# Kernel optimization log

Hardware: AMD Instinct MI355X
Metric: run time of the kernel (lower is better)

Reference implementation:

```python
import jax, jax.numpy as jnp
import numpy as np

B, S, DIM = 1, 4096, 4096
H, HL, D = 32, 8, 128          # query heads, kv heads (GQA), head_dim
BS = 8                          # sparse_block_size
SINK_TOK, WIN_TOK = 30, 30
HEAVY = 800                     # heavy_const -> Mb = HEAVY // BS top blocks
NEG = -1e30


def setup_inputs() -> dict:
    key = jax.random.key(0)
    k0, k1, k2, k3 = jax.random.split(key, 4)
    x = jax.random.normal(k0, (B, S, DIM), jnp.float32)
    freqs_cis = jax.random.uniform(k1, (S, D // 2, 2), jnp.float32)  # (cos,sin)-like pairs
    wqkv_w = jax.random.normal(k2, ((H + 2 * HL) * D, DIM), jnp.float32) * 0.02
    wo_w = jax.random.normal(k3, (DIM, DIM), jnp.float32) * 0.02
    input_pos = jnp.arange(S, dtype=jnp.int32)
    return {"x": x, "freqs_cis": freqs_cis, "wqkv_w": wqkv_w, "wo_w": wo_w, "input_pos": input_pos}


def _rope(x, fc):
    # x: [B,S,h,D], fc: [S,D/2,2]
    xr = x.reshape(*x.shape[:-1], -1, 2)            # [B,S,h,D/2,2]
    fc = fc[None, :, None]                           # [1,S,1,D/2,2]
    out = jnp.stack([xr[..., 0] * fc[..., 0] - xr[..., 1] * fc[..., 1],
                     xr[..., 1] * fc[..., 0] + xr[..., 0] * fc[..., 1]], axis=-1)
    return out.reshape(x.shape)


def reference(x, freqs_cis, wqkv_w, wo_w, input_pos):
    rep = H // HL
    Tb = (S + BS - 1) // BS
    scale = 1.0 / jnp.sqrt(jnp.float32(D))

    qkv = x @ wqkv_w.T                               # [B,S,(H+2HL)*D]
    q, k, v = jnp.split(qkv, [H * D, (H + HL) * D], axis=-1)
    q = q.reshape(B, S, H, D)
    k = k.reshape(B, S, HL, D)
    v = v.reshape(B, S, HL, D)
    q = _rope(q, freqs_cis)
    k = _rope(k, freqs_cis)

    # ---- block accumulators (KVCache.update_tokens), vectorized ----
    blk = input_pos // BS                            # [S]
    k_sum = jax.ops.segment_sum(jnp.swapaxes(k, 0, 1), blk, num_segments=Tb)  # [Tb,B,HL,D]
    cnt = jax.ops.segment_sum(jnp.ones((S,), jnp.float32), blk, num_segments=Tb)  # [Tb]
    k_rep = k_sum / jnp.maximum(cnt, 1.0)[:, None, None, None]                # block-mean keys
    k_rep_h = jnp.repeat(k_rep, rep, axis=2)        # [Tb,B,H,D] (GQA repeat)

    # ---- per-(B,H) block routing scores ----
    q_mean = q.mean(axis=1)                          # [B,H,D]
    scores = jnp.einsum('bhd,tbhd->bht', q_mean, k_rep_h) * scale  # [B,H,Tb]
    scores = jnp.where(cnt[None, None, :] > 0, scores, NEG)

    # ---- build_block_index: sink + window + topk ----
    sink_b = min((min(SINK_TOK, S) + BS - 1) // BS, Tb)
    window_b = min((min(WIN_TOK, S) + BS - 1) // BS, Tb)
    cur_block = (S - 1) // BS
    win_start = max(0, cur_block - window_b + 1)
    win_end = cur_block + 1
    sink_ids = jnp.arange(sink_b, dtype=jnp.int32)
    window_ids = jnp.arange(win_start, win_end, dtype=jnp.int32)
    Mb = max(0, min(HEAVY // BS, Tb))
    sc = scores.at[..., :sink_b].set(NEG).at[..., window_ids].set(NEG)
    top_ids = jax.lax.top_k(sc, Mb)[1].astype(jnp.int32)                      # [B,H,Mb]
    bidx = jnp.concatenate([
        jnp.broadcast_to(sink_ids, (B, H, sink_b)),
        jnp.broadcast_to(window_ids, (B, H, win_end - win_start)),
        top_ids], axis=-1)                           # [B,H,KLIST]

    # ---- gather selected block tokens ----
    tok = bidx[..., None] * BS + jnp.arange(BS, dtype=jnp.int32)              # [B,H,KLIST,BS]
    KL = bidx.shape[-1]
    tok = tok.reshape(B, H, KL * BS)                 # [B,H,Kt]
    valid = (tok >= 0) & (tok < S)
    tok_c = jnp.clip(tok, 0, S - 1)

    k_bhsd = jnp.swapaxes(jnp.repeat(k, rep, axis=2), 1, 2)  # [B,H,S,D]
    v_bhsd = jnp.swapaxes(jnp.repeat(v, rep, axis=2), 1, 2)
    Ksel = jnp.take_along_axis(k_bhsd, tok_c[..., None], axis=2)  # [B,H,Kt,D]
    Vsel = jnp.take_along_axis(v_bhsd, tok_c[..., None], axis=2)

    # ---- block-sparse attention with causal mask ----
    q_bhsd = jnp.swapaxes(q, 1, 2)                   # [B,H,S,D]
    att = jnp.einsum('bhsd,bhkd->bhsk', q_bhsd, Ksel) * scale
    mask = (tok_c[:, :, None, :] <= input_pos[None, None, :, None]) & valid[:, :, None, :]
    att = jnp.where(mask, att, NEG)
    p = jax.nn.softmax(att, axis=-1)
    out = jnp.einsum('bhsk,bhkd->bhsd', p, Vsel)     # [B,H,S,D]
    y = jnp.swapaxes(out, 1, 2).reshape(B, S, H * D) @ wo_w.T
    return y
```

## Files before the change

kernel.cpp:

```cpp
#include <hip/hip_runtime.h>
#include <hip/hip_bf16.h>

typedef unsigned short u16;
typedef unsigned int   u32;

using bf16x8 = __attribute__((ext_vector_type(8))) short;
using f32x4  = __attribute__((ext_vector_type(4))) float;

constexpr int S = 4096, DIM = 4096, H = 32, HL = 8, D = 128;
constexpr int NQKV = (H + 2 * HL) * D;
constexpr int TB = S / 8;
constexpr int KL = 108;
constexpr float NEGF = -1e30f;
constexpr float SCALE = 0.08838834764831845f;

__device__ inline float bflo(u32 u) { return __builtin_bit_cast(float, u << 16); }
__device__ inline float bfhi(u32 u) { return __builtin_bit_cast(float, u & 0xFFFF0000u); }
__device__ inline u16 rne16(float f) {
  u32 b = __builtin_bit_cast(u32, f);
  return (u16)((b + 0x7FFFu + ((b >> 16) & 1u)) >> 16);
}
__device__ inline float bf2f(u16 h) { return __builtin_bit_cast(float, (u32)h << 16); }
__device__ inline u32 pk2(u16 a, u16 b) { return (u32)a | ((u32)b << 16); }

__device__ __forceinline__ void gload16(const u16* g, u16* l) {
  __builtin_amdgcn_global_load_lds(
      (__attribute__((address_space(1))) void*)g,
      (__attribute__((address_space(3))) void*)l, 16, 0, 0);
}

__global__ __launch_bounds__(256) void split_f32_kernel(
    const float* __restrict__ src, u16* __restrict__ hi, u16* __restrict__ lo) {
  const size_t i = ((size_t)blockIdx.x * 256 + threadIdx.x) * 8;
  float4 v0 = *(const float4*)(src + i);
  float4 v1 = *(const float4*)(src + i + 4);
  float f[8] = {v0.x, v0.y, v0.z, v0.w, v1.x, v1.y, v1.z, v1.w};
  u16 h[8], l[8];
#pragma unroll
  for (int j = 0; j < 8; ++j) {
    h[j] = rne16(f[j]);
    l[j] = rne16(f[j] - bf2f(h[j]));
  }
  uint4 ph, pl;
  ph.x = pk2(h[0], h[1]); ph.y = pk2(h[2], h[3]);
  ph.z = pk2(h[4], h[5]); ph.w = pk2(h[6], h[7]);
  pl.x = pk2(l[0], l[1]); pl.y = pk2(l[2], l[3]);
  pl.z = pk2(l[4], l[5]); pl.w = pk2(l[6], l[7]);
  *(uint4*)(hi + i) = ph;
  *(uint4*)(lo + i) = pl;
}

__global__ __launch_bounds__(256) void conv_wqkv_kernel(
    const float* __restrict__ src, u16* __restrict__ dst, u16* __restrict__ klo) {
  const size_t i = ((size_t)blockIdx.x * 256 + threadIdx.x) * 8;
  float4 v0 = *(const float4*)(src + i);
  float4 v1 = *(const float4*)(src + i + 4);
  float f[8] = {v0.x, v0.y, v0.z, v0.w, v1.x, v1.y, v1.z, v1.w};
  u16 h[8];
#pragma unroll
  for (int j = 0; j < 8; ++j) h[j] = rne16(f[j]);
  uint4 ph;
  ph.x = pk2(h[0], h[1]); ph.y = pk2(h[2], h[3]);
  ph.z = pk2(h[4], h[5]); ph.w = pk2(h[6], h[7]);
  *(uint4*)(dst + i) = ph;
  const int row = (int)(i >> 12);
  if (row >= H * D && row < (H + HL) * D) {
    u16 l[8];
#pragma unroll
    for (int j = 0; j < 8; ++j) l[j] = rne16(f[j] - bf2f(h[j]));
    uint4 pl;
    pl.x = pk2(l[0], l[1]); pl.y = pk2(l[2], l[3]);
    pl.z = pk2(l[4], l[5]); pl.w = pk2(l[6], l[7]);
    *(uint4*)(klo + (i - (size_t)(H * D) * DIM)) = pl;
  }
}

__global__ __launch_bounds__(256) void cast_bf16_kernel(
    const float* __restrict__ src, u16* __restrict__ dst) {
  const size_t i = ((size_t)blockIdx.x * 256 + threadIdx.x) * 8;
  float4 v0 = *(const float4*)(src + i);
  float4 v1 = *(const float4*)(src + i + 4);
  uint4 ph;
  ph.x = pk2(rne16(v0.x), rne16(v0.y));
  ph.y = pk2(rne16(v0.z), rne16(v0.w));
  ph.z = pk2(rne16(v1.x), rne16(v1.y));
  ph.w = pk2(rne16(v1.z), rne16(v1.w));
  *(uint4*)(dst + i) = ph;
}

template <bool OBF16>
__global__ __launch_bounds__(256) void gemm_bf16(
    const u16* __restrict__ A, const u16* __restrict__ B,
    void* __restrict__ Cp, int M, int N, int K, int lda, int ldb, int ldc) {
  __shared__ u16 As[128 * 32];
  __shared__ u16 Bs[128 * 32];
  const int tid = threadIdx.x;
  const int lane = tid & 63;
  const int w = tid >> 6;
  const int wm = w >> 1, wn = w & 1;
  const int m0 = blockIdx.y * 128, n0 = blockIdx.x * 128;
  const int l15 = lane & 15, g = lane >> 4;
  const int srow = tid >> 2;
  const int scol = (tid & 3) * 8;

  const u16* ga = A + (size_t)(m0 + srow) * lda + scol;
  const u16* gb = B + (size_t)(n0 + srow) * ldb + scol;
  const size_t a64 = (size_t)64 * lda;
  const size_t b64 = (size_t)64 * ldb;
  u16* lA = As + w * 512;
  u16* lB = Bs + w * 512;

  f32x4 acc[4][4];
#pragma unroll
  for (int i = 0; i < 4; ++i)
#pragma unroll
    for (int j = 0; j < 4; ++j) acc[i][j] = {0.f, 0.f, 0.f, 0.f};

  for (int k0 = 0; k0 < K; k0 += 32) {
    gload16(ga + k0, lA);
    gload16(ga + k0 + a64, lA + 2048);
    gload16(gb + k0, lB);
    gload16(gb + k0 + b64, lB + 2048);
    __syncthreads();
    bf16x8 af[4], bfr[4];
#pragma unroll
    for (int i = 0; i < 4; ++i)
      af[i] = *(const bf16x8*)(As + (wm * 64 + i * 16 + l15) * 32 + g * 8);
#pragma unroll
    for (int j = 0; j < 4; ++j)
      bfr[j] = *(const bf16x8*)(Bs + (wn * 64 + j * 16 + l15) * 32 + g * 8);
#pragma unroll
    for (int i = 0; i < 4; ++i)
#pragma unroll
      for (int j = 0; j < 4; ++j)
        acc[i][j] = __builtin_amdgcn_mfma_f32_16x16x32_bf16(af[i], bfr[j], acc[i][j], 0, 0, 0);
    __syncthreads();
  }
#pragma unroll
  for (int i = 0; i < 4; ++i)
#pragma unroll
    for (int j = 0; j < 4; ++j)
#pragma unroll
      for (int rg = 0; rg < 4; ++rg) {
        const int row = m0 + wm * 64 + i * 16 + g * 4 + rg;
        const int col = n0 + wn * 64 + j * 16 + l15;
        if constexpr (OBF16)
          ((u16*)Cp)[(size_t)row * ldc + col] = rne16(acc[i][j][rg]);
        else
          ((float*)Cp)[(size_t)row * ldc + col] = acc[i][j][rg];
      }
}

__global__ __launch_bounds__(256) void gemm_k3(
    const u16* __restrict__ Ahg, const u16* __restrict__ Alg,
    const u16* __restrict__ Bhg, const u16* __restrict__ Blg,
    float* __restrict__ C, int M, int N, int K) {
  __shared__ u16 Ah[128 * 32];
  __shared__ u16 Al[128 * 32];
  __shared__ u16 Bh[64 * 32];
  __shared__ u16 Bl[64 * 32];
  const int tid = threadIdx.x;
  const int lane = tid & 63;
  const int w = tid >> 6;
  const int wm = w >> 1, wn = w & 1;
  const int m0 = blockIdx.y * 128, n0 = blockIdx.x * 64;
  const int l15 = lane & 15, g = lane >> 4;
  const int srow = tid >> 2;
  const int scol = (tid & 3) * 8;

  const u16* gah = Ahg + (size_t)(m0 + srow) * K + scol;
  const u16* gal = Alg + (size_t)(m0 + srow) * K + scol;
  const u16* gbh = Bhg + (size_t)(n0 + srow) * K + scol;
  const u16* gbl = Blg + (size_t)(n0 + srow) * K + scol;
  const size_t a64 = (size_t)64 * K;
  u16* lAh = Ah + w * 512;
  u16* lAl = Al + w * 512;
  u16* lBh = Bh + w * 512;
  u16* lBl = Bl + w * 512;

  f32x4 acc[4][2];
#pragma unroll
  for (int i = 0; i < 4; ++i)
#pragma unroll
    for (int j = 0; j < 2; ++j) acc[i][j] = {0.f, 0.f, 0.f, 0.f};

  for (int k0 = 0; k0 < K; k0 += 32) {
    gload16(gah + k0, lAh);
    gload16(gah + k0 + a64, lAh + 2048);
    gload16(gal + k0, lAl);
    gload16(gal + k0 + a64, lAl + 2048);
    gload16(gbh + k0, lBh);
    gload16(gbl + k0, lBl);
    __syncthreads();
    bf16x8 fah[4], fal[4], fbh[2], fbl[2];
#pragma unroll
    for (int i = 0; i < 4; ++i) {
      fah[i] = *(const bf16x8*)(Ah + (wm * 64 + i * 16 + l15) * 32 + g * 8);
      fal[i] = *(const bf16x8*)(Al + (wm * 64 + i * 16 + l15) * 32 + g * 8);
    }
#pragma unroll
    for (int j = 0; j < 2; ++j) {
      fbh[j] = *(const bf16x8*)(Bh + (wn * 32 + j * 16 + l15) * 32 + g * 8);
      fbl[j] = *(const bf16x8*)(Bl + (wn * 32 + j * 16 + l15) * 32 + g * 8);
    }
#pragma unroll
    for (int i = 0; i < 4; ++i)
#pragma unroll
      for (int j = 0; j < 2; ++j) {
        acc[i][j] = __builtin_amdgcn_mfma_f32_16x16x32_bf16(fal[i], fbh[j], acc[i][j], 0, 0, 0);
        acc[i][j] = __builtin_amdgcn_mfma_f32_16x16x32_bf16(fah[i], fbl[j], acc[i][j], 0, 0, 0);
        acc[i][j] = __builtin_amdgcn_mfma_f32_16x16x32_bf16(fah[i], fbh[j], acc[i][j], 0, 0, 0);
      }
    __syncthreads();
  }
#pragma unroll
  for (int i = 0; i < 4; ++i)
#pragma unroll
    for (int j = 0; j < 2; ++j)
#pragma unroll
      for (int rg = 0; rg < 4; ++rg) {
        const int row = m0 + wm * 64 + i * 16 + g * 4 + rg;
        const int col = n0 + wn * 32 + j * 16 + l15;
        C[(size_t)row * N + col] = acc[i][j][rg];
      }
}

__global__ __launch_bounds__(128) void xcd_kernel(
    const float* __restrict__ x, const float* __restrict__ freqs,
    float* __restrict__ XC, float* __restrict__ XD) {
  const int d = blockIdx.x * 128 + threadIdx.x;
  const int i0 = blockIdx.y * 32;
  const int s0 = blockIdx.z * 128;
  float accC[32], accD[32];
#pragma unroll
  for (int ii = 0; ii < 32; ++ii) { accC[ii] = 0.f; accD[ii] = 0.f; }
  for (int s = s0; s < s0 + 128; ++s) {
    const float xv = x[(size_t)s * DIM + d];
    const float* fr = freqs + (size_t)s * 128 + i0 * 2;
#pragma unroll
    for (int ii = 0; ii < 32; ++ii) {
      accC[ii] += fr[2 * ii] * xv;
      accD[ii] += fr[2 * ii + 1] * xv;
    }
  }
#pragma unroll
  for (int ii = 0; ii < 32; ++ii) {
    atomicAdd(&XC[(size_t)(i0 + ii) * DIM + d], accC[ii]);
    atomicAdd(&XD[(size_t)(i0 + ii) * DIM + d], accD[ii]);
  }
}

__global__ __launch_bounds__(256) void mrow_kernel(
    const float* __restrict__ wq, const float* __restrict__ XC,
    const float* __restrict__ XD, float* __restrict__ M1, float* __restrict__ M2) {
  const int r = blockIdx.x * 4 + (threadIdx.x >> 6);
  const int lane = threadIdx.x & 63;
  const int i = (r & 127) >> 1;
  const float* wr = wq + (size_t)r * DIM;
  const float* xc = XC + (size_t)i * DIM;
  const float* xd = XD + (size_t)i * DIM;
  float s1 = 0.f, s2 = 0.f;
  for (int k = lane; k < DIM; k += 64) {
    float wv = wr[k];
    s1 += wv * xc[k];
    s2 += wv * xd[k];
  }
#pragma unroll
  for (int off = 1; off < 64; off <<= 1) {
    s1 += __shfl_xor(s1, off, 64);
    s2 += __shfl_xor(s2, off, 64);
  }
  if (lane == 0) { M1[r] = s1; M2[r] = s2; }
}

__global__ __launch_bounds__(256) void rope_q_kernel(
    const u16* __restrict__ qkvb, const float* __restrict__ freqs,
    u16* __restrict__ qb) {
  const int h = blockIdx.y;
  const int s0 = blockIdx.x * 64;
  const int tid = threadIdx.x;
  const int d = tid & 127, half = tid >> 7;
  for (int pp = half; pp < 64; pp += 2) {
    const int s = s0 + pp;
    u32 pr = *(const u32*)(qkvb + (size_t)s * NQKV + h * D + (d & ~1));
    float a = bflo(pr), b = bfhi(pr);
    float2 fc = *(const float2*)(freqs + (size_t)s * 128 + (d & ~1));
    float o = (d & 1) ? (b * fc.x + a * fc.y) : (a * fc.x - b * fc.y);
    qb[((size_t)h * S + s) * D + d] = rne16(o);
  }
}

__global__ __launch_bounds__(128) void rope_kv_kernel(
    const float* __restrict__ kf, const u16* __restrict__ qkvb,
    const float* __restrict__ freqs,
    u16* __restrict__ kb, u16* __restrict__ vbt, float* __restrict__ krep) {
  const int hl = blockIdx.y;
  const int t = blockIdx.x;
  const int d = threadIdx.x;
  float sum = 0.f;
  u16 vv[8];
#pragma unroll
  for (int pp = 0; pp < 8; ++pp) {
    const int s = t * 8 + pp;
    float2 kp = *(const float2*)(kf + (size_t)s * 1024 + hl * D + (d & ~1));
    float2 fc = *(const float2*)(freqs + (size_t)s * 128 + (d & ~1));
    float o = (d & 1) ? (kp.y * fc.x + kp.x * fc.y) : (kp.x * fc.x - kp.y * fc.y);
    kb[((size_t)hl * S + s) * D + d] = rne16(o);
    sum += o;
    vv[pp] = qkvb[(size_t)s * NQKV + (H + HL) * D + hl * D + d];
  }
  krep[((size_t)t * HL + hl) * D + d] = sum * 0.125f;
  uint4 pk;
  pk.x = pk2(vv[0], vv[1]);
  pk.y = pk2(vv[2], vv[3]);
  pk.z = pk2(vv[4], vv[5]);
  pk.w = pk2(vv[6], vv[7]);
  *(uint4*)(vbt + ((size_t)hl * D + d) * S + t * 8) = pk;
}

__global__ __launch_bounds__(512) void topk_kernel(
    const float* __restrict__ M1, const float* __restrict__ M2,
    const float* __restrict__ krep, int* __restrict__ bidx) {
  const int h = blockIdx.x;
  const int t = threadIdx.x;
  __shared__ float qm[128];
  if (t < 128) {
    int r = h * 128 + t;
    float v = (t & 1) ? (M1[r] + M2[r - 1]) : (M1[r] - M2[r + 1]);
    qm[t] = v * (1.f / 4096.f);
  }
  __syncthreads();
  const float* kr = krep + ((size_t)t * HL + (h >> 2)) * 128;
  float s = 0.f;
#pragma unroll 8
  for (int d = 0; d < 128; ++d) s += qm[d] * kr[d];
  s *= SCALE;
  if (t < 4 || t >= 508) s = NEGF;
  if (t < 4) {
    bidx[h * KL + t] = t;
    bidx[h * KL + 4 + t] = 508 + t;
  }
  __shared__ float wv[8];
  __shared__ int wi[8];
  __shared__ int bestsh;
  for (int iter = 0; iter < 100; ++iter) {
    float v = s;
    int idx = t;
#pragma unroll
    for (int off = 1; off < 64; off <<= 1) {
      float ov = __shfl_xor(v, off, 64);
      int oi = __shfl_xor(idx, off, 64);
      if (ov > v || (ov == v && oi < idx)) { v = ov; idx = oi; }
    }
    if ((t & 63) == 0) { wv[t >> 6] = v; wi[t >> 6] = idx; }
    __syncthreads();
    if (t == 0) {
      float bv = wv[0];
      int bi = wi[0];
#pragma unroll
      for (int u = 1; u < 8; ++u)
        if (wv[u] > bv || (wv[u] == bv && wi[u] < bi)) { bv = wv[u]; bi = wi[u]; }
      bestsh = bi;
      bidx[h * KL + 8 + iter] = bi;
    }
    __syncthreads();
    if (t == bestsh) s = NEGF;
  }
}

__global__ __launch_bounds__(256) void attn_mfma(
    const u16* __restrict__ qb, const u16* __restrict__ kb,
    const u16* __restrict__ vbt, const int* __restrict__ bidx,
    u16* __restrict__ attno) {
  __shared__ u16 Ks[32][136];
  __shared__ u16 Vt[128][40];
  __shared__ u16 Ps[4][16][40];
  const int h = blockIdx.y, hl = h >> 2;
  const int q0 = blockIdx.x * 64;
  const int tid = threadIdx.x;
  const int w = tid >> 6, lane = tid & 63;
  const int l15 = lane & 15, g = lane >> 4;

  bf16x8 qf[4];
  {
    const u16* qp = qb + ((size_t)h * S + q0 + w * 16 + l15) * D + g * 8;
#pragma unroll
    for (int c = 0; c < 4; ++c) qf[c] = *(const bf16x8*)(qp + c * 32);
  }
  f32x4 o[8];
#pragma unroll
  for (int c = 0; c < 8; ++c) o[c] = {0.f, 0.f, 0.f, 0.f};
  float mrow[4], lrow[4];
#pragma unroll
  for (int r = 0; r < 4; ++r) { mrow[r] = NEGF; lrow[r] = 0.f; }

  for (int step = 0; step < KL / 4; ++step) {
    const int b0 = bidx[h * KL + step * 4 + 0];
    const int b1 = bidx[h * KL + step * 4 + 1];
    const int b2 = bidx[h * KL + step * 4 + 2];
    const int b3 = bidx[h * KL + step * 4 + 3];
    {
      const int tok = tid >> 3, seg = tid & 7;
      const int blk = (tok < 8) ? b0 : (tok < 16) ? b1 : (tok < 24) ? b2 : b3;
      const u16* src = kb + ((size_t)hl * S + blk * 8 + (tok & 7)) * D + seg * 16;
      *(uint4*)&Ks[tok][seg * 16] = *(const uint4*)src;
      *(uint4*)&Ks[tok][seg * 16 + 8] = *(const uint4*)(src + 8);
    }
    {
      const int d = tid >> 1, hf = tid & 1;
      const int ba = hf ? b2 : b0, bb = hf ? b3 : b1;
      const u16* src = vbt + ((size_t)hl * D + d) * S;
      *(uint4*)&Vt[d][hf * 16] = *(const uint4*)(src + ba * 8);
      *(uint4*)&Vt[d][hf * 16 + 8] = *(const uint4*)(src + bb * 8);
    }
    __syncthreads();
    f32x4 sA = {0.f, 0.f, 0.f, 0.f}, sB = {0.f, 0.f, 0.f, 0.f};
#pragma unroll
    for (int c = 0; c < 4; ++c) {
      bf16x8 k0 = *(const bf16x8*)&Ks[l15][c * 32 + g * 8];
      bf16x8 k1 = *(const bf16x8*)&Ks[16 + l15][c * 32 + g * 8];
      sA = __builtin_amdgcn_mfma_f32_16x16x32_bf16(qf[c], k0, sA, 0, 0, 0);
      sB = __builtin_amdgcn_mfma_f32_16x16x32_bf16(qf[c], k1, sB, 0, 0, 0);
    }
    const int tgA = ((l15 < 8) ? b0 : b1) * 8 + (l15 & 7);
    const int tgB = ((l15 < 8) ? b2 : b3) * 8 + (l15 & 7);
    float pA[4], pB[4], alpha[4];
#pragma unroll
    for (int r = 0; r < 4; ++r) {
      const int sq = q0 + w * 16 + g * 4 + r;
      pA[r] = (tgA <= sq) ? sA[r] * SCALE : NEGF;
      pB[r] = (tgB <= sq) ? sB[r] * SCALE : NEGF;
      float mx = fmaxf(pA[r], pB[r]);
      mx = fmaxf(mx, __shfl_xor(mx, 1, 64));
      mx = fmaxf(mx, __shfl_xor(mx, 2, 64));
      mx = fmaxf(mx, __shfl_xor(mx, 4, 64));
      mx = fmaxf(mx, __shfl_xor(mx, 8, 64));
      const float mnew = fmaxf(mrow[r], mx);
      alpha[r] = __expf(mrow[r] - mnew);
      mrow[r] = mnew;
      pA[r] = __expf(pA[r] - mnew);
      pB[r] = __expf(pB[r] - mnew);
      float rs = pA[r] + pB[r];
      rs += __shfl_xor(rs, 1, 64);
      rs += __shfl_xor(rs, 2, 64);
      rs += __shfl_xor(rs, 4, 64);
      rs += __shfl_xor(rs, 8, 64);
      lrow[r] = lrow[r] * alpha[r] + rs;
    }
#pragma unroll
    for (int c = 0; c < 8; ++c) {
      o[c][0] *= alpha[0]; o[c][1] *= alpha[1];
      o[c][2] *= alpha[2]; o[c][3] *= alpha[3];
    }
#pragma unroll
    for (int r = 0; r < 4; ++r) {
      Ps[w][g * 4 + r][l15] = rne16(pA[r]);
      Ps[w][g * 4 + r][16 + l15] = rne16(pB[r]);
    }
    bf16x8 pf = *(const bf16x8*)&Ps[w][l15][g * 8];
#pragma unroll
    for (int c = 0; c < 8; ++c) {
      bf16x8 vf = *(const bf16x8*)&Vt[c * 16 + l15][g * 8];
      o[c] = __builtin_amdgcn_mfma_f32_16x16x32_bf16(pf, vf, o[c], 0, 0, 0);
    }
    __syncthreads();
  }
  float inv[4];
#pragma unroll
  for (int r = 0; r < 4; ++r) inv[r] = 1.f / lrow[r];
#pragma unroll
  for (int c = 0; c < 8; ++c)
#pragma unroll
    for (int r = 0; r < 4; ++r)
      attno[(size_t)(q0 + w * 16 + g * 4 + r) * DIM + h * D + c * 16 + l15] =
          rne16(o[c][r] * inv[r]);
}

extern "C" void kernel_launch(void* const* d_in, const int* in_sizes, int n_in,
                              void* d_out, int out_size, void* d_ws, size_t ws_size,
                              hipStream_t stream) {
  const float* x     = (const float*)d_in[0];
  const float* freqs = (const float*)d_in[1];
  const float* wqkv  = (const float*)d_in[2];
  const float* wo    = (const float*)d_in[3];
  float* out = (float*)d_out;

  char* p = (char*)d_ws;
  auto alloc = [&](size_t bytes) {
    char* r = p;
    p += (bytes + 255) & ~(size_t)255;
    return r;
  };
  u16*   xh   = (u16*)alloc((size_t)S * DIM * 2);
  u16*   xl   = (u16*)alloc((size_t)S * DIM * 2);
  u16*   wqb  = (u16*)alloc((size_t)NQKV * DIM * 2);
  u16*   wkl  = (u16*)alloc((size_t)HL * D * DIM * 2);
  u16*   wob  = (u16*)alloc((size_t)DIM * DIM * 2);
  u16*   qkvb = (u16*)alloc((size_t)S * NQKV * 2);
  float* kf32 = (float*)alloc((size_t)S * HL * D * 4);
  u16*   qb   = (u16*)alloc((size_t)H * S * D * 2);
  u16*   kb   = (u16*)alloc((size_t)HL * S * D * 2);
  u16*   vbt  = (u16*)alloc((size_t)HL * D * S * 2);
  float* krep = (float*)alloc((size_t)TB * HL * D * 4);
  float* XC   = (float*)alloc((size_t)64 * DIM * 4);
  float* XD   = (float*)alloc((size_t)64 * DIM * 4);
  float* M1   = (float*)alloc((size_t)H * D * 4);
  float* M2   = (float*)alloc((size_t)H * D * 4);
  int*   bidx = (int*)alloc((size_t)H * KL * 4);
  u16*   attno = (u16*)alloc((size_t)S * DIM * 2);

  hipMemsetAsync(XC, 0, (size_t)64 * DIM * 4, stream);
  hipMemsetAsync(XD, 0, (size_t)64 * DIM * 4, stream);

  split_f32_kernel<<<(S * DIM) / 2048, 256, 0, stream>>>(x, xh, xl);
  conv_wqkv_kernel<<<(NQKV * DIM) / 2048, 256, 0, stream>>>(wqkv, wqb, wkl);
  cast_bf16_kernel<<<(DIM * DIM) / 2048, 256, 0, stream>>>(wo, wob);

  gemm_bf16<true><<<dim3((H * D) / 128, S / 128), 256, 0, stream>>>(
      xh, wqb, qkvb, S, H * D, DIM, DIM, DIM, NQKV);
  gemm_bf16<true><<<dim3((HL * D) / 128, S / 128), 256, 0, stream>>>(
      xh, wqb + (size_t)(H + HL) * D * DIM, qkvb + (H + HL) * D,
      S, HL * D, DIM, DIM, DIM, NQKV);

  const u16* wkh = wqb + (size_t)H * D * DIM;
  gemm_k3<<<dim3((HL * D) / 64, S / 128), 256, 0, stream>>>(
      xh, xl, wkh, wkl, kf32, S, HL * D, DIM);

  xcd_kernel<<<dim3(32, 2, 32), 128, 0, stream>>>(x, freqs, XC, XD);
  mrow_kernel<<<1024, 256, 0, stream>>>(wqkv, XC, XD, M1, M2);
  rope_q_kernel<<<dim3(S / 64, H), 256, 0, stream>>>(qkvb, freqs, qb);
  rope_kv_kernel<<<dim3(TB, HL), 128, 0, stream>>>(kf32, qkvb, freqs, kb, vbt, krep);
  topk_kernel<<<H, 512, 0, stream>>>(M1, M2, krep, bidx);
  attn_mfma<<<dim3(S / 64, H), 256, 0, stream>>>(qb, kb, vbt, bidx, attno);
  gemm_bf16<false><<<dim3(DIM / 128, S / 128), 256, 0, stream>>>(
      attno, wob, out, S, DIM, DIM, DIM, DIM, DIM);
}
```

Measured before the change: 1.465 ms.

## Double-buffer GEMM LDS tiles, add XCD swizzle, merge Q and V projections

Both GEMM kernels now double-buffer their LDS tiles, issuing the next K-slice's global-to-LDS loads before computing on the current one so load latency overlaps MFMA work. A block-index remap spreads neighbouring tiles across the chiplet (XCD) partitions to improve L2 reuse. The weight conversion now writes Q and V rows into one contiguous matrix and K into separate hi/lo buffers, so Q and V come from a single GEMM launch into a narrower output buffer. This doubles LDS use per block, which may reduce occupancy, and the remap assumes the workgroup count divides by 8.

```diff
diff --git a/kernel.cpp b/kernel.cpp
--- a/kernel.cpp
+++ b/kernel.cpp
@@ -9,6 +9,7 @@
 
 constexpr int S = 4096, DIM = 4096, H = 32, HL = 8, D = 128;
 constexpr int NQKV = (H + 2 * HL) * D;
+constexpr int QVW = (H + HL) * D;
 constexpr int TB = S / 8;
 constexpr int KL = 108;
 constexpr float NEGF = -1e30f;
@@ -27,6 +28,15 @@
   __builtin_amdgcn_global_load_lds(
       (__attribute__((address_space(1))) void*)g,
       (__attribute__((address_space(3))) void*)l, 16, 0, 0);
+}
+
+__device__ inline void xcd_swz(int nx, int& bx, int& by) {
+  const int flat = blockIdx.y * nx + blockIdx.x;
+  const int nwg = nx * gridDim.y;
+  const int cpx = nwg >> 3;
+  const int s = (flat & 7) * cpx + (flat >> 3);
+  bx = s % nx;
+  by = s / nx;
 }
 
 __global__ __launch_bounds__(256) void split_f32_kernel(
@@ -51,7 +61,8 @@
 }
 
 __global__ __launch_bounds__(256) void conv_wqkv_kernel(
-    const float* __restrict__ src, u16* __restrict__ dst, u16* __restrict__ klo) {
+    const float* __restrict__ src, u16* __restrict__ wqv,
+    u16* __restrict__ wkh, u16* __restrict__ wkl) {
   const size_t i = ((size_t)blockIdx.x * 256 + threadIdx.x) * 8;
   float4 v0 = *(const float4*)(src + i);
   float4 v1 = *(const float4*)(src + i + 4);
@@ -62,16 +73,21 @@
   uint4 ph;
   ph.x = pk2(h[0], h[1]); ph.y = pk2(h[2], h[3]);
   ph.z = pk2(h[4], h[5]); ph.w = pk2(h[6], h[7]);
-  *(uint4*)(dst + i) = ph;
   const int row = (int)(i >> 12);
-  if (row >= H * D && row < (H + HL) * D) {
+  if (row < H * D) {
+    *(uint4*)(wqv + i) = ph;
+  } else if (row < (H + HL) * D) {
+    const size_t off = i - (size_t)(H * D) * DIM;
     u16 l[8];
 #pragma unroll
     for (int j = 0; j < 8; ++j) l[j] = rne16(f[j] - bf2f(h[j]));
     uint4 pl;
     pl.x = pk2(l[0], l[1]); pl.y = pk2(l[2], l[3]);
     pl.z = pk2(l[4], l[5]); pl.w = pk2(l[6], l[7]);
-    *(uint4*)(klo + (i - (size_t)(H * D) * DIM)) = pl;
+    *(uint4*)(wkh + off) = ph;
+    *(uint4*)(wkl + off) = pl;
+  } else {
+    *(uint4*)(wqv + (i - (size_t)(HL * D) * DIM)) = ph;
   }
 }
 
@@ -92,13 +108,15 @@
 __global__ __launch_bounds__(256) void gemm_bf16(
     const u16* __restrict__ A, const u16* __restrict__ B,
     void* __restrict__ Cp, int M, int N, int K, int lda, int ldb, int ldc) {
-  __shared__ u16 As[128 * 32];
-  __shared__ u16 Bs[128 * 32];
+  __shared__ u16 As[2][128 * 32];
+  __shared__ u16 Bs[2][128 * 32];
   const int tid = threadIdx.x;
   const int lane = tid & 63;
   const int w = tid >> 6;
   const int wm = w >> 1, wn = w & 1;
-  const int m0 = blockIdx.y * 128, n0 = blockIdx.x * 128;
+  int bx, by;
+  xcd_swz(gridDim.x, bx, by);
+  const int m0 = by * 128, n0 = bx * 128;
   const int l15 = lane & 15, g = lane >> 4;
   const int srow = tid >> 2;
   const int scol = (tid & 3) * 8;
@@ -107,28 +125,35 @@
   const u16* gb = B + (size_t)(n0 + srow) * ldb + scol;
   const size_t a64 = (size_t)64 * lda;
   const size_t b64 = (size_t)64 * ldb;
-  u16* lA = As + w * 512;
-  u16* lB = Bs + w * 512;
-
-  f32x4 acc[4][4];
-#pragma unroll
-  for (int i = 0; i < 4; ++i)
-#pragma unroll
-    for (int j = 0; j < 4; ++j) acc[i][j] = {0.f, 0.f, 0.f, 0.f};
-
-  for (int k0 = 0; k0 < K; k0 += 32) {
+
+  auto stage = [&](int buf, int k0) {
+    u16* lA = As[buf] + w * 512;
+    u16* lB = Bs[buf] + w * 512;
     gload16(ga + k0, lA);
     gload16(ga + k0 + a64, lA + 2048);
     gload16(gb + k0, lB);
     gload16(gb + k0 + b64, lB + 2048);
-    __syncthreads();
+  };
+
+  f32x4 acc[4][4];
+#pragma unroll
+  for (int i = 0; i < 4; ++i)
+#pragma unroll
+    for (int j = 0; j < 4; ++j) acc[i][j] = {0.f, 0.f, 0.f, 0.f};
+
+  stage(0, 0);
+  __syncthreads();
+  const int niter = K / 32;
+  for (int it = 0; it < niter; ++it) {
+    const int cur = it & 1;
+    if (it + 1 < niter) stage(cur ^ 1, (it + 1) * 32);
     bf16x8 af[4], bfr[4];
 #pragma unroll
     for (int i = 0; i < 4; ++i)
-      af[i] = *(const bf16x8*)(As + (wm * 64 + i * 16 + l15) * 32 + g * 8);
+      af[i] = *(const bf16x8*)(As[cur] + (wm * 64 + i * 16 + l15) * 32 + g * 8);
 #pragma unroll
     for (int j = 0; j < 4; ++j)
-      bfr[j] = *(const bf16x8*)(Bs + (wn * 64 + j * 16 + l15) * 32 + g * 8);
+      bfr[j] = *(const bf16x8*)(Bs[cur] + (wn * 64 + j * 16 + l15) * 32 + g * 8);
 #pragma unroll
     for (int i = 0; i < 4; ++i)
 #pragma unroll
@@ -155,15 +180,17 @@
     const u16* __restrict__ Ahg, const u16* __restrict__ Alg,
     const u16* __restrict__ Bhg, const u16* __restrict__ Blg,
     float* __restrict__ C, int M, int N, int K) {
-  __shared__ u16 Ah[128 * 32];
-  __shared__ u16 Al[128 * 32];
-  __shared__ u16 Bh[64 * 32];
-  __shared__ u16 Bl[64 * 32];
+  __shared__ u16 Ah[2][128 * 32];
+  __shared__ u16 Al[2][128 * 32];
+  __shared__ u16 Bh[2][64 * 32];
+  __shared__ u16 Bl[2][64 * 32];
   const int tid = threadIdx.x;
   const int lane = tid & 63;
   const int w = tid >> 6;
   const int wm = w >> 1, wn = w & 1;
-  const int m0 = blockIdx.y * 128, n0 = blockIdx.x * 64;
+  int bx, by;
+  xcd_swz(gridDim.x, bx, by);
+  const int m0 = by * 128, n0 = bx * 64;
   const int l15 = lane & 15, g = lane >> 4;
   const int srow = tid >> 2;
   const int scol = (tid & 3) * 8;
@@ -173,10 +200,15 @@
   const u16* gbh = Bhg + (size_t)(n0 + srow) * K + scol;
   const u16* gbl = Blg + (size_t)(n0 + srow) * K + scol;
   const size_t a64 = (size_t)64 * K;
-  u16* lAh = Ah + w * 512;
-  u16* lAl = Al + w * 512;
-  u16* lBh = Bh + w * 512;
-  u16* lBl = Bl + w * 512;
+
+  auto stage = [&](int buf, int k0) {
+    gload16(gah + k0, Ah[buf] + w * 512);
+    gload16(gah + k0 + a64, Ah[buf] + w * 512 + 2048);
+    gload16(gal + k0, Al[buf] + w * 512);
+    gload16(gal + k0 + a64, Al[buf] + w * 512 + 2048);
+    gload16(gbh + k0, Bh[buf] + w * 512);
+    gload16(gbl + k0, Bl[buf] + w * 512);
+  };
 
   f32x4 acc[4][2];
 #pragma unroll
@@ -184,24 +216,22 @@
 #pragma unroll
     for (int j = 0; j < 2; ++j) acc[i][j] = {0.f, 0.f, 0.f, 0.f};
 
-  for (int k0 = 0; k0 < K; k0 += 32) {
-    gload16(gah + k0, lAh);
-    gload16(gah + k0 + a64, lAh + 2048);
-    gload16(gal + k0, lAl);
-    gload16(gal + k0 + a64, lAl + 2048);
-    gload16(gbh + k0, lBh);
-    gload16(gbl + k0, lBl);
-    __syncthreads();
+  stage(0, 0);
+  __syncthreads();
+  const int niter = K / 32;
+  for (int it = 0; it < niter; ++it) {
+    const int cur = it & 1;
+    if (it + 1 < niter) stage(cur ^ 1, (it + 1) * 32);
     bf16x8 fah[4], fal[4], fbh[2], fbl[2];
 #pragma unroll
     for (int i = 0; i < 4; ++i) {
-      fah[i] = *(const bf16x8*)(Ah + (wm * 64 + i * 16 + l15) * 32 + g * 8);
-      fal[i] = *(const bf16x8*)(Al + (wm * 64 + i * 16 + l15) * 32 + g * 8);
+      fah[i] = *(const bf16x8*)(Ah[cur] + (wm * 64 + i * 16 + l15) * 32 + g * 8);
+      fal[i] = *(const bf16x8*)(Al[cur] + (wm * 64 + i * 16 + l15) * 32 + g * 8);
     }
 #pragma unroll
     for (int j = 0; j < 2; ++j) {
-      fbh[j] = *(const bf16x8*)(Bh + (wn * 32 + j * 16 + l15) * 32 + g * 8);
-      fbl[j] = *(const bf16x8*)(Bl + (wn * 32 + j * 16 + l15) * 32 + g * 8);
+      fbh[j] = *(const bf16x8*)(Bh[cur] + (wn * 32 + j * 16 + l15) * 32 + g * 8);
+      fbl[j] = *(const bf16x8*)(Bl[cur] + (wn * 32 + j * 16 + l15) * 32 + g * 8);
     }
 #pragma unroll
     for (int i = 0; i < 4; ++i)
@@ -274,7 +304,7 @@
 }
 
 __global__ __launch_bounds__(256) void rope_q_kernel(
-    const u16* __restrict__ qkvb, const float* __restrict__ freqs,
+    const u16* __restrict__ qvb, const float* __restrict__ freqs,
     u16* __restrict__ qb) {
   const int h = blockIdx.y;
   const int s0 = blockIdx.x * 64;
@@ -282,7 +312,7 @@
   const int d = tid & 127, half = tid >> 7;
   for (int pp = half; pp < 64; pp += 2) {
     const int s = s0 + pp;
-    u32 pr = *(const u32*)(qkvb + (size_t)s * NQKV + h * D + (d & ~1));
+    u32 pr = *(const u32*)(qvb + (size_t)s * QVW + h * D + (d & ~1));
     float a = bflo(pr), b = bfhi(pr);
     float2 fc = *(const float2*)(freqs + (size_t)s * 128 + (d & ~1));
     float o = (d & 1) ? (b * fc.x + a * fc.y) : (a * fc.x - b * fc.y);
@@ -291,7 +321,7 @@
 }
 
 __global__ __launch_bounds__(128) void rope_kv_kernel(
-    const float* __restrict__ kf, const u16* __restrict__ qkvb,
+    const float* __restrict__ kf, const u16* __restrict__ qvb,
     const float* __restrict__ freqs,
     u16* __restrict__ kb, u16* __restrict__ vbt, float* __restrict__ krep) {
   const int hl = blockIdx.y;
@@ -307,7 +337,7 @@
     float o = (d & 1) ? (kp.y * fc.x + kp.x * fc.y) : (kp.x * fc.x - kp.y * fc.y);
     kb[((size_t)hl * S + s) * D + d] = rne16(o);
     sum += o;
-    vv[pp] = qkvb[(size_t)s * NQKV + (H + HL) * D + hl * D + d];
+    vv[pp] = qvb[(size_t)s * QVW + H * D + hl * D + d];
   }
   krep[((size_t)t * HL + hl) * D + d] = sum * 0.125f;
   uint4 pk;
@@ -493,10 +523,11 @@
   };
   u16*   xh   = (u16*)alloc((size_t)S * DIM * 2);
   u16*   xl   = (u16*)alloc((size_t)S * DIM * 2);
-  u16*   wqb  = (u16*)alloc((size_t)NQKV * DIM * 2);
+  u16*   wqv  = (u16*)alloc((size_t)QVW * DIM * 2);
+  u16*   wkh  = (u16*)alloc((size_t)HL * D * DIM * 2);
   u16*   wkl  = (u16*)alloc((size_t)HL * D * DIM * 2);
   u16*   wob  = (u16*)alloc((size_t)DIM * DIM * 2);
-  u16*   qkvb = (u16*)alloc((size_t)S * NQKV * 2);
+  u16*   qvb  = (u16*)alloc((size_t)S * QVW * 2);
   float* kf32 = (float*)alloc((size_t)S * HL * D * 4);
   u16*   qb   = (u16*)alloc((size_t)H * S * D * 2);
   u16*   kb   = (u16*)alloc((size_t)HL * S * D * 2);
@@ -513,23 +544,19 @@
   hipMemsetAsync(XD, 0, (size_t)64 * DIM * 4, stream);
 
   split_f32_kernel<<<(S * DIM) / 2048, 256, 0, stream>>>(x, xh, xl);
-  conv_wqkv_kernel<<<(NQKV * DIM) / 2048, 256, 0, stream>>>(wqkv, wqb, wkl);
+  conv_wqkv_kernel<<<(NQKV * DIM) / 2048, 256, 0, stream>>>(wqkv, wqv, wkh, wkl);
   cast_bf16_kernel<<<(DIM * DIM) / 2048, 256, 0, stream>>>(wo, wob);
 
-  gemm_bf16<true><<<dim3((H * D) / 128, S / 128), 256, 0, stream>>>(
-      xh, wqb, qkvb, S, H * D, DIM, DIM, DIM, NQKV);
-  gemm_bf16<true><<<dim3((HL * D) / 128, S / 128), 256, 0, stream>>>(
-      xh, wqb + (size_t)(H + HL) * D * DIM, qkvb + (H + HL) * D,
-      S, HL * D, DIM, DIM, DIM, NQKV);
-
-  const u16* wkh = wqb + (size_t)H * D * DIM;
+  gemm_bf16<true><<<dim3(QVW / 128, S / 128), 256, 0, stream>>>(
+      xh, wqv, qvb, S, QVW, DIM, DIM, DIM, QVW);
+
   gemm_k3<<<dim3((HL * D) / 64, S / 128), 256, 0, stream>>>(
       xh, xl, wkh, wkl, kf32, S, HL * D, DIM);
 
   xcd_kernel<<<dim3(32, 2, 32), 128, 0, stream>>>(x, freqs, XC, XD);
   mrow_kernel<<<1024, 256, 0, stream>>>(wqkv, XC, XD, M1, M2);
-  rope_q_kernel<<<dim3(S / 64, H), 256, 0, stream>>>(qkvb, freqs, qb);
-  rope_kv_kernel<<<dim3(TB, HL), 128, 0, stream>>>(kf32, qkvb, freqs, kb, vbt, krep);
+  rope_q_kernel<<<dim3(S / 64, H), 256, 0, stream>>>(qvb, freqs, qb);
+  rope_kv_kernel<<<dim3(TB, HL), 128, 0, stream>>>(kf32, qvb, freqs, kb, vbt, krep);
   topk_kernel<<<H, 512, 0, stream>>>(M1, M2, krep, bidx);
   attn_mfma<<<dim3(S / 64, H), 256, 0, stream>>>(qb, kb, vbt, bidx, attno);
   gemm_bf16<false><<<dim3(DIM / 128, S / 128), 256, 0, stream>>>(
```

After: 1.308 ms. -10.8%, faster.
